# Performance work log

Measured on AMD Instinct MI355X. Metric: run time of the kernel, lower is better.

## Reference

```python
import jax, jax.numpy as jnp
import numpy as np

HQ, HKV, D, NE = 8, 2, 48, 384   # query heads, kv heads, head_size, n_embd
GROUP = HQ // HKV                # query heads per kv head (repeat_interleave factor)
ROPE_BASE = 10000
NEG_INF = -1e30


def rope_cache(T, head_dim):
    # matches build_rope_cache: inv_freq over even indices, angles = pos * inv_freq
    inv_freq = 1.0 / (ROPE_BASE ** (jnp.arange(0, head_dim, 2, dtype=jnp.float32) / head_dim))
    pos = jnp.arange(T, dtype=jnp.float32)
    ang = pos[:, None] * inv_freq[None, :]          # [T, D/2]
    return jnp.cos(ang), jnp.sin(ang)


def apply_rope(x, cos, sin):
    # interleaved (even/odd) rotation, re-interleaved via stack+reshape
    xe = x[..., 0::2]
    xo = x[..., 1::2]
    re = xe * cos - xo * sin
    ro = xe * sin + xo * cos
    return jnp.stack((re, ro), axis=-1).reshape(x.shape)


def setup_inputs() -> dict:
    key = jax.random.key(0)
    ks = jax.random.split(key, 6)
    B, T = 8, 2048
    s = lambda n: 1.0 / np.sqrt(n)
    return {
        "x":  jax.random.normal(ks[0], (B, T, NE), jnp.float32),
        "wq": jax.random.normal(ks[1], (NE, HQ * D), jnp.float32) * s(NE),
        "wk": jax.random.normal(ks[2], (NE, HKV * D), jnp.float32) * s(NE),
        "wv": jax.random.normal(ks[3], (NE, HKV * D), jnp.float32) * s(NE),
        "wo": jax.random.normal(ks[4], (NE, NE), jnp.float32) * s(NE),
        "bo": jnp.zeros((NE,), jnp.float32),
    }


def reference(x, wq, wk, wv, wo, bo):
    B, T, _ = x.shape
    # QKV projections (weights stored [in, out]); [B, H, T, D]
    q = (x @ wq).reshape(B, T, HQ, D).transpose(0, 2, 1, 3)
    k = (x @ wk).reshape(B, T, HKV, D).transpose(0, 2, 1, 3)
    v = (x @ wv).reshape(B, T, HKV, D).transpose(0, 2, 1, 3)

    cos, sin = rope_cache(T, D)                      # [T, D/2]
    cos = cos[None, None]                            # [1,1,T,D/2]
    sin = sin[None, None]
    q = apply_rope(q, cos, sin)
    k = apply_rope(k, cos, sin)

    # GQA: group query heads per kv head (math-identical to repeat_interleave on k/v)
    qg = q.reshape(B, HKV, GROUP, T, D)
    scale = 1.0 / np.sqrt(D)
    scores = jnp.einsum('bhgtd,bhsd->bhgts', qg, k) * scale   # [B,HKV,G,T,T]
    causal = jnp.tril(jnp.ones((T, T), dtype=bool))
    scores = jnp.where(causal, scores, NEG_INF)
    attn = jax.nn.softmax(scores, axis=-1)
    out = jnp.einsum('bhgts,bhsd->bhgtd', attn, v)            # [B,HKV,G,T,D]
    out = out.reshape(B, HQ, T, D).transpose(0, 2, 1, 3).reshape(B, T, NE)
    # output projection (eval mode: dropout is identity)
    return out @ wo + bo
```

## Files before the change

### kernel.cpp

```cpp
#include <hip/hip_runtime.h>
#include <math.h>

#define B_   8
#define T_   2048
#define NE_  384
#define HQ_  8
#define HKV_ 2
#define D_   48
#define DH_  24

typedef __attribute__((ext_vector_type(8))) short bf16x8;
typedef __attribute__((ext_vector_type(4))) short bf16x4;
typedef __attribute__((ext_vector_type(4))) float f32x4;

static __device__ __forceinline__ short f2bf(float f) {
    union { float f; unsigned u; } v; v.f = f;
    unsigned r = (v.u + 0x7fffu + ((v.u >> 16) & 1u)) >> 16;
    return (short)r;
}

static __device__ __forceinline__ float exp2_fast(float x) {
    float r;
    asm("v_exp_f32 %0, %1" : "=v"(r) : "v"(x));
    return r;
}
static __device__ __forceinline__ unsigned cvt_pk_bf16(float lo, float hi) {
    unsigned r;
    asm("v_cvt_pk_bf16_f32 %0, %1, %2" : "=v"(r) : "v"(lo), "v"(hi));
    return r;
}
static __device__ __forceinline__ float max3f(float a, float b, float c) {
    float r;
    asm("v_max3_f32 %0, %1, %2, %3" : "=v"(r) : "v"(a), "v"(b), "v"(c));
    return r;
}
static __device__ __forceinline__ void gld16(const void* g, void* l) {
    __builtin_amdgcn_global_load_lds(
        (const __attribute__((address_space(1))) unsigned int*)g,
        (__attribute__((address_space(3))) unsigned int*)l,
        16, 0, 0);
}

__global__ __launch_bounds__(256) void prep_kernel(
    const float* __restrict__ x, const float* __restrict__ wq,
    const float* __restrict__ wk, const float* __restrict__ wv,
    const float* __restrict__ wo,
    short* __restrict__ xb, short* __restrict__ wt, short* __restrict__ wot,
    float* __restrict__ ct, float* __restrict__ st)
{
    const int bid = blockIdx.x, tid = threadIdx.x;
    if (bid < 6144) {
        int i = bid * 256 + tid;
        float4 v = ((const float4*)x)[i];
        bf16x4 o = { f2bf(v.x), f2bf(v.y), f2bf(v.z), f2bf(v.w) };
        *(bf16x4*)&xb[(size_t)i * 4] = o;
    } else if (bid < 7008) {
        int e = (bid - 6144) * 256 + tid;
        int n = e / 384, k = e - n * 384;
        float s = (n < 384) ? wq[(size_t)k * 384 + n]
                : (n < 480) ? wk[(size_t)k * 96 + (n - 384)]
                            : wv[(size_t)k * 96 + (n - 480)];
        wt[e] = f2bf(s);
    } else if (bid < 7584) {
        int e = (bid - 7008) * 256 + tid;
        int n = e / 384, k = e - n * 384;
        wot[e] = f2bf(wo[(size_t)k * 384 + n]);
    } else {
        int i = (bid - 7584) * 256 + tid;
        int t = i / DH_, j = i - t * DH_;
        double inv = pow(10000.0, -(double)(2 * j) / (double)D_);
        double ang = (double)t * inv;
        ct[i] = (float)cos(ang);
        st[i] = (float)sin(ang);
    }
}

__global__ __launch_bounds__(256) void qkv_gemm_kernel(
    const short* __restrict__ xb, const short* __restrict__ wt,
    const float* __restrict__ ct, const float* __restrict__ st,
    short* __restrict__ qb, short* __restrict__ kb, short* __restrict__ vtb)
{
    __shared__ __align__(16) char ldsb[49152];
    const int tid = threadIdx.x;
    const int n0 = blockIdx.x * 64;
    const int m0 = blockIdx.y * 128;
    const int lane = tid & 63, w = tid >> 6;
    const int c = lane & 15, u = lane >> 4;
    const int mo = (w & 1) * 64, no = (w >> 1) * 32;
    const int lrow = lane >> 3;
    const int lcol = (((lane & 7) ^ lrow) << 4);
    f32x4 acc[4][2] = {};

    auto stage = [&](int bsel, int t) {
        char* dst = ldsb + bsel * 24576;
        const char* Ag = (const char*)xb + (size_t)(m0 + w * 32 + lrow) * 768 + t * 128 + lcol;
#pragma unroll
        for (int p = 0; p < 4; ++p)
            gld16(Ag + p * 8 * 768, dst + w * 4096 + p * 1024);
        const char* Bg = (const char*)wt + (size_t)(n0 + w * 16 + lrow) * 768 + t * 128 + lcol;
#pragma unroll
        for (int p = 0; p < 2; ++p)
            gld16(Bg + p * 8 * 768, dst + 16384 + w * 2048 + p * 1024);
    };

    stage(0, 0);
    __syncthreads();
    int cur = 0;
#pragma unroll 1
    for (int t = 0; t < 6; ++t) {
        if (t < 5) stage(cur ^ 1, t + 1);
        const char* Ab = ldsb + cur * 24576;
        const char* Bb = Ab + 16384;
#pragma unroll
        for (int kk = 0; kk < 2; ++kk) {
            const int off = (kk * 64 + u * 16) ^ ((c & 7) << 4);
            bf16x8 af[4], bfr[2];
#pragma unroll
            for (int i = 0; i < 4; ++i)
                af[i] = *(const bf16x8*)(Ab + (mo + 16 * i + c) * 128 + off);
#pragma unroll
            for (int j = 0; j < 2; ++j)
                bfr[j] = *(const bf16x8*)(Bb + (no + 16 * j + c) * 128 + off);
#pragma unroll
            for (int i = 0; i < 4; ++i)
#pragma unroll
                for (int j = 0; j < 2; ++j)
                    acc[i][j] = __builtin_amdgcn_mfma_f32_16x16x32_bf16(af[i], bfr[j], acc[i][j], 0, 0, 0);
        }
        __syncthreads();
        cur ^= 1;
    }

    const float qscale = 0.14433756729740643f * 1.4426950408889634f;
#pragma unroll
    for (int i = 0; i < 4; ++i) {
#pragma unroll
        for (int j = 0; j < 2; ++j) {
            int n = n0 + no + 16 * j + c;
            int mb = m0 + mo + 16 * i + 4 * u;
            int b = mb >> 11;
            int t0 = mb & 2047;
            if (n < 480) {
                int nn = (n < 384) ? n : n - 384;
                int h = nn / 48, d = nn - h * 48;
                int fi = d >> 1;
                float sgn = (d & 1) ? 1.0f : -1.0f;
                float scl = (n < 384) ? qscale : 1.0f;
                short* dst = (n < 384) ? qb : kb;
                size_t base = (n < 384)
                    ? ((size_t)(b * HQ_ + h) * T_ + t0) * 64 + d
                    : ((size_t)(b * HKV_ + h) * T_ + t0) * 64 + d;
#pragma unroll
                for (int r = 0; r < 4; ++r) {
                    float val = acc[i][j][r];
                    float part = __shfl_xor(val, 1);
                    float cs = ct[(t0 + r) * DH_ + fi], sn = st[(t0 + r) * DH_ + fi];
                    dst[base + (size_t)r * 64] = f2bf((val * cs + sgn * part * sn) * scl);
                }
            } else {
                int nn = n - 480;
                int h = nn / 48, d = nn - h * 48;
                ushort4 pk;
                pk.x = (unsigned short)f2bf(acc[i][j][0]);
                pk.y = (unsigned short)f2bf(acc[i][j][1]);
                pk.z = (unsigned short)f2bf(acc[i][j][2]);
                pk.w = (unsigned short)f2bf(acc[i][j][3]);
                *(ushort4*)&vtb[((size_t)(b * HKV_ + h) * D_ + d) * T_ + t0] = pk;
            }
        }
    }
}

__global__ __launch_bounds__(256, 2) void attn_kernel(
    const short* __restrict__ qb, const short* __restrict__ kb,
    const short* __restrict__ vtb, short* __restrict__ aob)
{
    __shared__ __align__(16) short lds_s[14336];
    const int tid = threadIdx.x;
    const int x  = blockIdx.x;
    const int hk = blockIdx.y >> 1;
    const int gp = blockIdx.y & 1;
    const int b  = blockIdx.z;
    const int lane = tid & 63;
    const int w = tid >> 6;
    const int c = lane & 15;
    const int u = lane >> 4;
    const int qt0 = 31 - x;
    const int qt1 = x;

    const char* kg = (const char*)kb  + (size_t)(b * HKV_ + hk) * T_ * 128;
    const char* vg = (const char*)vtb + (size_t)(b * HKV_ + hk) * D_ * T_ * 2;

    const int swz  = (lane ^ ((lane >> 3) & 7)) << 4;
    const int vrow = lane >> 3;
    const int voff = swz & 127;

    const int mk  = (c & 7) << 4;
    const int okl = (u * 16) ^ mk;
    const int okh = (64 | (u * 16)) ^ mk;

    auto stage = [&](int bsel, int jt) {
        char* dst = (char*)lds_s + bsel * 14336;
        const char* kt = kg + (size_t)jt * 8192;
        gld16(kt + (2 * w) * 1024 + swz,     dst + (2 * w) * 1024);
        gld16(kt + (2 * w + 1) * 1024 + swz, dst + (2 * w + 1) * 1024);
        if (w < 3) {
            const char* vt = vg + (size_t)jt * 128;
            gld16(vt + (size_t)(16 * w + vrow) * 4096 + voff,
                  dst + 8192 + (2 * w) * 1024);
            gld16(vt + (size_t)(16 * w + 8 + vrow) * 4096 + voff,
                  dst + 8192 + (2 * w + 1) * 1024);
        }
    };

    bf16x8 qf0[2][2], qf1[2][2];
#pragma unroll
    for (int qs = 0; qs < 2; ++qs) {
        const int qt = qs ? qt1 : qt0;
#pragma unroll
        for (int g = 0; g < 2; ++g) {
            int h = hk * 4 + gp * 2 + g;
            const short* qp = qb + ((size_t)(b * HQ_ + h) * T_ + qt * 64 + 16 * w + c) * 64;
            qf0[qs][g] = *(const bf16x8*)(qp + 8 * u);
            qf1[qs][g] = *(const bf16x8*)(qp + 32 + 8 * u);
        }
    }
    float m_s[2][2] = { { -1e30f, -1e30f }, { -1e30f, -1e30f } };
    float l_s[2][2] = {};
    f32x4 o[2][2][3] = {};

    int cur = 0;
    stage(0, 0);
    __syncthreads();

#pragma unroll 1
    for (int jt = 0; jt <= qt0; ++jt) {
        if (jt < qt0) stage(cur ^ 1, jt + 1);

        const int fmax = (jt == qt0) ? (w + 1) : 4;
        const char* kbuf = (const char*)lds_s + cur * 14336;
        const char* vbuf = kbuf + 8192;

        bf16x8 klo[4], khi[4];
        bf16x4 vf[3][4];
#pragma unroll
        for (int mt = 0; mt < 4; ++mt) {
            if (mt < fmax) {
                klo[mt] = *(const bf16x8*)(kbuf + mt * 2048 + c * 128 + okl);
                khi[mt] = *(const bf16x8*)(kbuf + mt * 2048 + c * 128 + okh);
            }
        }
#pragma unroll
        for (int nt = 0; nt < 3; ++nt)
#pragma unroll
            for (int k2 = 0; k2 < 4; ++k2)
                if (k2 < fmax)
                    vf[nt][k2] = *(const bf16x4*)(vbuf + nt * 2048 + c * 128 +
                                                  (((k2 * 32) | (u * 8)) ^ mk));

#pragma unroll
        for (int qs = 0; qs < 2; ++qs) {
            const int qt = qs ? qt1 : qt0;
            if (qs == 1 && jt > qt1) continue;
            const bool diag = (jt == qt);
            const int mtmax = diag ? (w + 1) : 4;

#pragma unroll
            for (int g = 0; g < 2; ++g) {
                f32x4 s[4];
                __builtin_amdgcn_s_setprio(1);
#pragma unroll
                for (int mt = 0; mt < 4; ++mt) {
                    if (mt < mtmax) {
                        f32x4 a = {0.f, 0.f, 0.f, 0.f};
                        a = __builtin_amdgcn_mfma_f32_16x16x32_bf16(klo[mt], qf0[qs][g], a, 0, 0, 0);
                        a = __builtin_amdgcn_mfma_f32_16x16x32_bf16(khi[mt], qf1[qs][g], a, 0, 0, 0);
                        if (diag && mt == mtmax - 1) {
#pragma unroll
                            for (int r = 0; r < 4; ++r)
                                a[r] = (4 * u + r > c) ? -1e30f : a[r];
                        }
                        s[mt] = a;
                    }
                }
                __builtin_amdgcn_s_setprio(0);

                float mloc = -1e30f;
#pragma unroll
                for (int mt = 0; mt < 4; ++mt)
                    if (mt < mtmax)
                        mloc = max3f(max3f(s[mt][0], s[mt][1], s[mt][2]), s[mt][3], mloc);
                mloc = fmaxf(mloc, __shfl_xor(mloc, 16));
                mloc = fmaxf(mloc, __shfl_xor(mloc, 32));

                if (__any(mloc > m_s[qs][g] + 8.0f)) {
                    float mnew = fmaxf(m_s[qs][g], mloc);
                    float alpha = exp2_fast(m_s[qs][g] - mnew);
                    m_s[qs][g] = mnew;
                    l_s[qs][g] *= alpha;
                    float a0 = __shfl(alpha, 4 * u + 0);
                    float a1 = __shfl(alpha, 4 * u + 1);
                    float a2 = __shfl(alpha, 4 * u + 2);
                    float a3 = __shfl(alpha, 4 * u + 3);
#pragma unroll
                    for (int nt = 0; nt < 3; ++nt) {
                        o[qs][g][nt][0] *= a0; o[qs][g][nt][1] *= a1;
                        o[qs][g][nt][2] *= a2; o[qs][g][nt][3] *= a3;
                    }
                }

                float psum = 0.0f;
                bf16x4 pf[4];
#pragma unroll
                for (int mt = 0; mt < 4; ++mt) {
                    if (mt < mtmax) {
                        float p0 = exp2_fast(s[mt][0] - m_s[qs][g]);
                        float p1 = exp2_fast(s[mt][1] - m_s[qs][g]);
                        float p2 = exp2_fast(s[mt][2] - m_s[qs][g]);
                        float p3 = exp2_fast(s[mt][3] - m_s[qs][g]);
                        psum += (p0 + p1) + (p2 + p3);
                        union { unsigned u2[2]; bf16x4 v; } pk;
                        pk.u2[0] = cvt_pk_bf16(p0, p1);
                        pk.u2[1] = cvt_pk_bf16(p2, p3);
                        pf[mt] = pk.v;
                    }
                }
                psum += __shfl_xor(psum, 16);
                psum += __shfl_xor(psum, 32);
                l_s[qs][g] += psum;

                __builtin_amdgcn_s_setprio(1);
#pragma unroll
                for (int k2 = 0; k2 < 4; ++k2) {
                    if (k2 < mtmax) {
#pragma unroll
                        for (int nt = 0; nt < 3; ++nt)
                            o[qs][g][nt] = __builtin_amdgcn_mfma_f32_16x16x16bf16_1k(
                                pf[k2], vf[nt][k2], o[qs][g][nt], 0, 0, 0);
                    }
                }
                __builtin_amdgcn_s_setprio(0);
            }
        }

        __syncthreads();
        cur ^= 1;
    }

#pragma unroll
    for (int qs = 0; qs < 2; ++qs) {
        const int qt = qs ? qt1 : qt0;
#pragma unroll
        for (int g = 0; g < 2; ++g) {
            int h = hk * 4 + gp * 2 + g;
            float li = 1.0f / l_s[qs][g];
            float l0 = __shfl(li, 4 * u + 0);
            float l1 = __shfl(li, 4 * u + 1);
            float l2 = __shfl(li, 4 * u + 2);
            float l3 = __shfl(li, 4 * u + 3);
            float lr[4] = { l0, l1, l2, l3 };
#pragma unroll
            for (int nt = 0; nt < 3; ++nt)
#pragma unroll
                for (int r = 0; r < 4; ++r) {
                    int t = qt * 64 + 16 * w + 4 * u + r;
                    aob[((size_t)b * T_ + t) * NE_ + h * D_ + 16 * nt + c] =
                        f2bf(o[qs][g][nt][r] * lr[r]);
                }
        }
    }
}

__global__ __launch_bounds__(256) void out_gemm_kernel(
    const short* __restrict__ aob, const short* __restrict__ wot,
    const float* __restrict__ bias, float* __restrict__ out)
{
    __shared__ __align__(16) char ldsb[49152];
    const int tid = threadIdx.x;
    const int n0 = blockIdx.x * 64;
    const int m0 = blockIdx.y * 128;
    const int lane = tid & 63, w = tid >> 6;
    const int c = lane & 15, u = lane >> 4;
    const int mo = (w & 1) * 64, no = (w >> 1) * 32;
    const int lrow = lane >> 3;
    const int lcol = (((lane & 7) ^ lrow) << 4);
    f32x4 acc[4][2] = {};

    auto stage = [&](int bsel, int t) {
        char* dst = ldsb + bsel * 24576;
        const char* Ag = (const char*)aob + (size_t)(m0 + w * 32 + lrow) * 768 + t * 128 + lcol;
#pragma unroll
        for (int p = 0; p < 4; ++p)
            gld16(Ag + p * 8 * 768, dst + w * 4096 + p * 1024);
        const char* Bg = (const char*)wot + (size_t)(n0 + w * 16 + lrow) * 768 + t * 128 + lcol;
#pragma unroll
        for (int p = 0; p < 2; ++p)
            gld16(Bg + p * 8 * 768, dst + 16384 + w * 2048 + p * 1024);
    };

    stage(0, 0);
    __syncthreads();
    int cur = 0;
#pragma unroll 1
    for (int t = 0; t < 6; ++t) {
        if (t < 5) stage(cur ^ 1, t + 1);
        const char* Ab = ldsb + cur * 24576;
        const char* Bb = Ab + 16384;
#pragma unroll
        for (int kk = 0; kk < 2; ++kk) {
            const int off = (kk * 64 + u * 16) ^ ((c & 7) << 4);
            bf16x8 af[4], bfr[2];
#pragma unroll
            for (int i = 0; i < 4; ++i)
                af[i] = *(const bf16x8*)(Ab + (mo + 16 * i + c) * 128 + off);
#pragma unroll
            for (int j = 0; j < 2; ++j)
                bfr[j] = *(const bf16x8*)(Bb + (no + 16 * j + c) * 128 + off);
#pragma unroll
            for (int i = 0; i < 4; ++i)
#pragma unroll
                for (int j = 0; j < 2; ++j)
                    acc[i][j] = __builtin_amdgcn_mfma_f32_16x16x32_bf16(af[i], bfr[j], acc[i][j], 0, 0, 0);
        }
        __syncthreads();
        cur ^= 1;
    }

#pragma unroll
    for (int i = 0; i < 4; ++i) {
#pragma unroll
        for (int j = 0; j < 2; ++j) {
            int n = n0 + no + 16 * j + c;
            int mb = m0 + mo + 16 * i + 4 * u;
            float bv = bias[n];
#pragma unroll
            for (int r = 0; r < 4; ++r)
                out[(size_t)(mb + r) * 384 + n] = acc[i][j][r] + bv;
        }
    }
}

extern "C" void kernel_launch(void* const* d_in, const int* in_sizes, int n_in,
                              void* d_out, int out_size, void* d_ws, size_t ws_size,
                              hipStream_t stream) {
    const float* x  = (const float*)d_in[0];
    const float* wq = (const float*)d_in[1];
    const float* wk = (const float*)d_in[2];
    const float* wv = (const float*)d_in[3];
    const float* wo = (const float*)d_in[4];
    const float* bo = (const float*)d_in[5];
    float* out = (float*)d_out;

    float* ct  = (float*)d_ws;
    float* st  = ct + 49152;
    short* xb  = (short*)(st + 49152);
    short* wt  = xb  + (size_t)16384 * 384;
    short* wot = wt  + (size_t)576 * 384;
    short* qb  = wot + (size_t)384 * 384;
    short* kb  = qb  + (size_t)B_ * HQ_  * T_ * 64;
    short* vtb = kb  + (size_t)B_ * HKV_ * T_ * 64;
    short* aob = vtb + (size_t)B_ * HKV_ * D_ * T_;

    hipLaunchKernelGGL(prep_kernel, dim3(7776), dim3(256), 0, stream,
                       x, wq, wk, wv, wo, xb, wt, wot, ct, st);
    hipMemsetAsync(qb, 0, ((size_t)B_ * HQ_ * T_ * 64 + (size_t)B_ * HKV_ * T_ * 64) * sizeof(short), stream);
    hipLaunchKernelGGL(qkv_gemm_kernel, dim3(9, 128), dim3(256), 0, stream,
                       xb, wt, ct, st, qb, kb, vtb);
    hipLaunchKernelGGL(attn_kernel, dim3(16, 4, 8), dim3(256), 0, stream,
                       qb, kb, vtb, aob);
    hipLaunchKernelGGL(out_gemm_kernel, dim3(6, 128), dim3(256), 0, stream,
                       aob, wot, bo, out);
}
```

Measured before the change: 206.3 us.

## Zero only padding columns in prep kernel, defer row-sum reduction, use float rope

Replaces the full-buffer memset of the padded q/k buffers with extra prep-kernel blocks that zero only the 16 padding columns per row. This cuts memset traffic and one launch. The attention kernel now keeps per-lane partial row sums and does the cross-lane shuffle reduction once at the end, removing two shuffles per tile. The rope table is computed with float powf/__sincosf instead of double, which may slightly reduce accuracy for large angles.

```diff
diff --git a/kernel.cpp b/kernel.cpp
--- a/kernel.cpp
+++ b/kernel.cpp
@@ -46,7 +46,8 @@
     const float* __restrict__ wk, const float* __restrict__ wv,
     const float* __restrict__ wo,
     short* __restrict__ xb, short* __restrict__ wt, short* __restrict__ wot,
-    float* __restrict__ ct, float* __restrict__ st)
+    float* __restrict__ ct, float* __restrict__ st,
+    short* __restrict__ qb)
 {
     const int bid = blockIdx.x, tid = threadIdx.x;
     if (bid < 6144) {
@@ -65,13 +66,20 @@
         int e = (bid - 7008) * 256 + tid;
         int n = e / 384, k = e - n * 384;
         wot[e] = f2bf(wo[(size_t)k * 384 + n]);
-    } else {
+    } else if (bid < 7776) {
         int i = (bid - 7584) * 256 + tid;
         int t = i / DH_, j = i - t * DH_;
-        double inv = pow(10000.0, -(double)(2 * j) / (double)D_);
-        double ang = (double)t * inv;
-        ct[i] = (float)cos(ang);
-        st[i] = (float)sin(ang);
+        float inv = powf(10000.0f, -(float)(2 * j) / (float)D_);
+        float ang = (float)t * inv;
+        float sv, cv;
+        __sincosf(ang, &sv, &cv);
+        ct[i] = cv;
+        st[i] = sv;
+    } else {
+        int i = (bid - 7776) * 256 + tid;
+        int row = i >> 1, half = i & 1;
+        bf16x8 z = {};
+        *(bf16x8*)&qb[(size_t)row * 64 + 48 + half * 8] = z;
     }
 }
 
@@ -309,7 +317,6 @@
                     }
                 }
 
-                float psum = 0.0f;
                 bf16x4 pf[4];
 #pragma unroll
                 for (int mt = 0; mt < 4; ++mt) {
@@ -318,16 +325,13 @@
                         float p1 = exp2_fast(s[mt][1] - m_s[qs][g]);
                         float p2 = exp2_fast(s[mt][2] - m_s[qs][g]);
                         float p3 = exp2_fast(s[mt][3] - m_s[qs][g]);
-                        psum += (p0 + p1) + (p2 + p3);
+                        l_s[qs][g] += (p0 + p1) + (p2 + p3);
                         union { unsigned u2[2]; bf16x4 v; } pk;
                         pk.u2[0] = cvt_pk_bf16(p0, p1);
                         pk.u2[1] = cvt_pk_bf16(p2, p3);
                         pf[mt] = pk.v;
                     }
                 }
-                psum += __shfl_xor(psum, 16);
-                psum += __shfl_xor(psum, 32);
-                l_s[qs][g] += psum;
 
                 __builtin_amdgcn_s_setprio(1);
 #pragma unroll
@@ -353,7 +357,10 @@
 #pragma unroll
         for (int g = 0; g < 2; ++g) {
             int h = hk * 4 + gp * 2 + g;
-            float li = 1.0f / l_s[qs][g];
+            float lt = l_s[qs][g];
+            lt += __shfl_xor(lt, 16);
+            lt += __shfl_xor(lt, 32);
+            float li = 1.0f / lt;
             float l0 = __shfl(li, 4 * u + 0);
             float l1 = __shfl(li, 4 * u + 1);
             float l2 = __shfl(li, 4 * u + 2);
@@ -461,9 +468,8 @@
     short* vtb = kb  + (size_t)B_ * HKV_ * T_ * 64;
     short* aob = vtb + (size_t)B_ * HKV_ * D_ * T_;
 
-    hipLaunchKernelGGL(prep_kernel, dim3(7776), dim3(256), 0, stream,
-                       x, wq, wk, wv, wo, xb, wt, wot, ct, st);
-    hipMemsetAsync(qb, 0, ((size_t)B_ * HQ_ * T_ * 64 + (size_t)B_ * HKV_ * T_ * 64) * sizeof(short), stream);
+    hipLaunchKernelGGL(prep_kernel, dim3(9056), dim3(256), 0, stream,
+                       x, wq, wk, wv, wo, xb, wt, wot, ct, st, qb);
     hipLaunchKernelGGL(qkv_gemm_kernel, dim3(9, 128), dim3(256), 0, stream,
                        xb, wt, ct, st, qb, kb, vtb);
     hipLaunchKernelGGL(attn_kernel, dim3(16, 4, 8), dim3(256), 0, stream,
```

New measurement: 199.5 us. -3.3%, faster.
